# Kernel optimization log

Hardware: AMD Instinct MI355X
Metric: run time of the kernel (lower is better)

## Reference

```python
import jax, jax.numpy as jnp
import numpy as np

B, S, D = 2, 512, 128      # batch, seq_len, d_att
DG, NG = 64, 2             # d_group, n_group = D // DG


def setup_inputs() -> dict:
    key = jax.random.key(0)
    ks = jax.random.split(key, 12)
    def w(k, shape, scale):
        return jax.random.normal(k, shape, dtype=jnp.float32) * scale
    proj_scale = 1.0 / D                      # xavier_uniform-ish std / sqrt(d_att)
    mlp1 = (2.0 / (DG + DG)) ** 0.5
    mlp2 = (2.0 / (DG + 16)) ** 0.5
    mlp3 = (2.0 / (16 + 1)) ** 0.5
    return {
        "x": w(ks[0], (B, S, D), 1.0),
        "positional_adding_bias": w(ks[1], (1, NG, 1, S, S), 1.0),
        "positional_multiplying_bias": jax.random.uniform(ks[2], (1, NG, 1, S, S), dtype=jnp.float32),
        "Wq": w(ks[3], (D, D), proj_scale),
        "Wk": w(ks[4], (D, D), proj_scale),
        "Wv": w(ks[5], (D, D), proj_scale),
        "W1": w(ks[6], (DG, DG), mlp1), "b1": jnp.zeros((DG,), jnp.float32),
        "W2": w(ks[7], (DG, 16), mlp2), "b2": jnp.zeros((16,), jnp.float32),
        "W3": w(ks[8], (16, 1), mlp3),  "b3": jnp.zeros((1,), jnp.float32),
    }


def reference(x, positional_adding_bias, positional_multiplying_bias,
              Wq, Wk, Wv, W1, b1, W2, b2, W3, b3):
    Q = x @ Wq   # [B,S,D]
    K = x @ Wk
    V = x @ Wv
    # pairwise Q-K differences, grouped: [B,S,S,NG,DG] (d_att split as n_group,d_group)
    diff = (Q[:, :, None, :] - K[:, None, :, :]).reshape(B, S, S, NG, DG)
    # per-group scoring MLP (Linear->ReLU x3, final width 1)
    h = jax.nn.relu(diff @ W1 + b1)
    h = jax.nn.relu(h @ W2 + b2)
    a = jax.nn.relu(h @ W3 + b3)                 # [B,S,S,NG,1]
    a = jnp.transpose(a, (0, 3, 4, 1, 2))        # [B,NG,1,S,S]
    a = a * positional_multiplying_bias + positional_adding_bias
    a = jax.nn.softmax(a, axis=-1)[:, :, 0]      # [B,NG,S,S], softmax over keys
    # NOTE: original reshapes V as (d_group, n_group) — faithful reproduction
    Vr = V.reshape(B, S, DG, NG)                 # [B,S,DG,NG]
    out = jnp.einsum('bisk,bkji->bsji', a, Vr)   # [B,S,DG,NG]
    return out.reshape(B, S, D)
```

## Files before the change

kernel.cpp:

```cpp
#include <hip/hip_runtime.h>

#define BQ 2
#define SQ 512
#define DQ 128
#define DGQ 64
#define NGQ 2

typedef float float2v __attribute__((ext_vector_type(2)));


__global__ __launch_bounds__(256) void proj_kernel(
    const float* __restrict__ x,
    const float* __restrict__ Wq, const float* __restrict__ Wk,
    const float* __restrict__ Wv,
    const float* __restrict__ W1, const float* __restrict__ b1,
    float* __restrict__ QW1, float* __restrict__ KW1, float* __restrict__ Vp)
{
    const int t = threadIdx.x;
    const int row = blockIdx.x;
    __shared__ float xs[DQ];
    __shared__ float part[3][2][DQ];
    __shared__ float qs[DQ], ks[DQ];

    if (t < DQ) xs[t] = x[(size_t)row * DQ + t];
    __syncthreads();

    const int f = t & 127, h = t >> 7;
    float aq = 0.f, ak = 0.f, av = 0.f;
    const int d0 = h * 64;
    #pragma unroll 8
    for (int d = 0; d < 64; ++d) {
        const float xv = xs[d0 + d];
        const size_t o = (size_t)(d0 + d) * DQ + f;
        aq = fmaf(xv, Wq[o], aq);
        ak = fmaf(xv, Wk[o], ak);
        av = fmaf(xv, Wv[o], av);
    }
    part[0][h][f] = aq; part[1][h][f] = ak; part[2][h][f] = av;
    __syncthreads();

    if (t < DQ) {
        qs[t] = part[0][0][t] + part[0][1][t];
        const float v = part[2][0][t] + part[2][1][t];
        Vp[((size_t)row * NGQ + (t & 1)) * DGQ + (t >> 1)] = v;
    } else {
        const int f2 = t - DQ;
        ks[f2] = part[1][0][f2] + part[1][1][f2];
    }
    __syncthreads();

    const int fb = t & 127, side = t >> 7;
    const int g = fb >> 6, c = fb & 63;
    const float* src = side ? ks : qs;
    float acc = side ? 0.f : b1[c];
    #pragma unroll 8
    for (int e = 0; e < 64; ++e)
        acc = fmaf(src[g * 64 + e], W1[e * DGQ + c], acc);
    (side ? KW1 : QW1)[(size_t)row * DQ + fb] = acc;
}

__global__ __launch_bounds__(512) void attn_kernel(
    const float* __restrict__ QW1, const float* __restrict__ KW1,
    const float* __restrict__ Vp,
    const float* __restrict__ W2, const float* __restrict__ b2,
    const float* __restrict__ W3, const float* __restrict__ b3,
    const float* __restrict__ pos_add, const float* __restrict__ pos_mul,
    float* __restrict__ out)
{
    const int t = threadIdx.x;
    const int ipair = blockIdx.x & 255;
    const int g = (blockIdx.x >> 8) & 1;
    const int b = blockIdx.x >> 9;
    const int i0 = ipair * 2;

    __shared__ __align__(16) float qsl[2][DGQ];
    __shared__ __align__(8)  float sc[SQ * 2];
    __shared__ float redm[2][8], reds[2][8];
    __shared__ float avs[2][8][DGQ];

    if (t < 2 * DGQ) {
        const int qq = t >> 6, e = t & 63;
        qsl[qq][e] = QW1[((size_t)(b * SQ + i0 + qq)) * DQ + g * DGQ + e];
    }
    const size_t bo0 = ((size_t)g * SQ + i0) * SQ + t;
    const float pm0 = pos_mul[bo0],      pa0 = pos_add[bo0];
    const float pm1 = pos_mul[bo0 + SQ], pa1 = pos_add[bo0 + SQ];
    __syncthreads();

    const float4* krow = reinterpret_cast<const float4*>(
        KW1 + ((size_t)(b * SQ + t)) * DQ + g * DGQ);
    const float4* qv0 = reinterpret_cast<const float4*>(&qsl[0][0]);
    const float4* qv1 = reinterpret_cast<const float4*>(&qsl[1][0]);
    const float2v* b2v = reinterpret_cast<const float2v*>(b2);
    const float2v zero2 = {0.f, 0.f};

    float2v acc0[8], acc1[8];
    #pragma unroll
    for (int o = 0; o < 8; ++o) { acc0[o] = b2v[o]; acc1[o] = b2v[o]; }

    float4 kva = krow[0], kvb = krow[1];
    #pragma unroll
    for (int grp = 0; grp < 8; ++grp) {
        float4 nka, nkb;
        if (grp < 7) { nka = krow[grp * 2 + 2]; nkb = krow[grp * 2 + 3]; }
        #pragma unroll
        for (int u = 0; u < 2; ++u) {
            const int c4 = grp * 2 + u;
            const float4 kv = u ? kvb : kva;
            const float4 qa = qv0[c4], qb = qv1[c4];
            const float2v k01 = {kv.x, kv.y}, k23 = {kv.z, kv.w};
            const float2v ha01 = __builtin_elementwise_max(
                float2v{qa.x, qa.y} - k01, zero2);
            const float2v ha23 = __builtin_elementwise_max(
                float2v{qa.z, qa.w} - k23, zero2);
            const float2v hb01 = __builtin_elementwise_max(
                float2v{qb.x, qb.y} - k01, zero2);
            const float2v hb23 = __builtin_elementwise_max(
                float2v{qb.z, qb.w} - k23, zero2);
            const float2v* w2r = reinterpret_cast<const float2v*>(W2 + c4 * 64);
            #pragma unroll
            for (int o = 0; o < 8; ++o) {
                const float2v w0 = w2r[o],      w1 = w2r[8 + o];
                const float2v w2_ = w2r[16 + o], w3_ = w2r[24 + o];
                acc0[o] += ha01.x * w0;  acc0[o] += ha01.y * w1;
                acc0[o] += ha23.x * w2_; acc0[o] += ha23.y * w3_;
                acc1[o] += hb01.x * w0;  acc1[o] += hb01.y * w1;
                acc1[o] += hb23.x * w2_; acc1[o] += hb23.y * w3_;
            }
        }
        kva = nka; kvb = nkb;
    }
    float a0 = b3[0], a1 = b3[0];
    #pragma unroll
    for (int o = 0; o < 8; ++o) {
        a0 = fmaf(fmaxf(acc0[o].x, 0.f), W3[2 * o], a0);
        a0 = fmaf(fmaxf(acc0[o].y, 0.f), W3[2 * o + 1], a0);
        a1 = fmaf(fmaxf(acc1[o].x, 0.f), W3[2 * o], a1);
        a1 = fmaf(fmaxf(acc1[o].y, 0.f), W3[2 * o + 1], a1);
    }
    const float logit0 = fmaf(fmaxf(a0, 0.f), pm0, pa0);
    const float logit1 = fmaf(fmaxf(a1, 0.f), pm1, pa1);

    float m0 = logit0, m1 = logit1;
    #pragma unroll
    for (int off = 32; off > 0; off >>= 1) {
        m0 = fmaxf(m0, __shfl_xor(m0, off));
        m1 = fmaxf(m1, __shfl_xor(m1, off));
    }
    const int wave = t >> 6;
    if ((t & 63) == 0) { redm[0][wave] = m0; redm[1][wave] = m1; }
    __syncthreads();
    float M0 = redm[0][0], M1 = redm[1][0];
    #pragma unroll
    for (int w = 1; w < 8; ++w) {
        M0 = fmaxf(M0, redm[0][w]); M1 = fmaxf(M1, redm[1][w]);
    }
    const float e0 = __expf(logit0 - M0);
    const float e1 = __expf(logit1 - M1);
    *reinterpret_cast<float2v*>(&sc[t * 2]) = float2v{e0, e1};
    float s0 = e0, s1 = e1;
    #pragma unroll
    for (int off = 32; off > 0; off >>= 1) {
        s0 += __shfl_xor(s0, off);
        s1 += __shfl_xor(s1, off);
    }
    if ((t & 63) == 0) { reds[0][wave] = s0; reds[1][wave] = s1; }
    __syncthreads();
    float S0 = 0.f, S1 = 0.f;
    #pragma unroll
    for (int w = 0; w < 8; ++w) { S0 += reds[0][w]; S1 += reds[1][w]; }
    const float inv0 = 1.f / S0, inv1 = 1.f / S1;

    const int dim = t & 63, q = t >> 6;
    const float* vbase = Vp + (((size_t)(b * SQ + q * 64)) * NGQ + g) * DGQ + dim;
    float2v accv = {0.f, 0.f};
    #pragma unroll 16
    for (int k = 0; k < 64; ++k) {
        const float v = vbase[(size_t)k * (NGQ * DGQ)];
        const float2v sv = *reinterpret_cast<const float2v*>(&sc[(q * 64 + k) * 2]);
        accv += v * sv;
    }
    avs[0][q][dim] = accv.x;
    avs[1][q][dim] = accv.y;
    __syncthreads();
    if (t < 2 * DGQ) {
        const int qq = t >> 6, d = t & 63;
        float sum = 0.f;
        #pragma unroll
        for (int w = 0; w < 8; ++w) sum += avs[qq][w][d];
        out[((size_t)(b * SQ + i0 + qq)) * DQ + d * NGQ + g] =
            sum * (qq ? inv1 : inv0);
    }
}

extern "C" void kernel_launch(void* const* d_in, const int* in_sizes, int n_in,
                              void* d_out, int out_size, void* d_ws, size_t ws_size,
                              hipStream_t stream) {
    const float* x       = (const float*)d_in[0];
    const float* pos_add = (const float*)d_in[1];
    const float* pos_mul = (const float*)d_in[2];
    const float* Wq      = (const float*)d_in[3];
    const float* Wk      = (const float*)d_in[4];
    const float* Wv      = (const float*)d_in[5];
    const float* W1      = (const float*)d_in[6];
    const float* b1      = (const float*)d_in[7];
    const float* W2      = (const float*)d_in[8];
    const float* b2      = (const float*)d_in[9];
    const float* W3      = (const float*)d_in[10];
    const float* b3      = (const float*)d_in[11];
    float* out = (float*)d_out;

    float* ws  = (float*)d_ws;
    float* QW1 = ws;
    float* KW1 = ws + 131072;
    float* Vp  = ws + 262144;

    proj_kernel<<<BQ * SQ, 256, 0, stream>>>(x, Wq, Wk, Wv, W1, b1,
                                             QW1, KW1, Vp);
    attn_kernel<<<BQ * NGQ * SQ / 2, 512, 0, stream>>>(QW1, KW1, Vp, W2, b2,
                                                       W3, b3, pos_add, pos_mul,
                                                       out);
}
```

Before: 118.7 us.

## Compute scoring MLP layer 2 with split-bf16 MFMA and four queries per block

Replaces the per-thread scalar FMA evaluation of the 64->16 MLP layer with 16x16x32 bf16 MFMA instructions. A three-term hi/lo bf16 split keeps near-fp32 accuracy. Each block now handles four query rows instead of two, so K rows and W2 fragments are reused across more queries, and the grid shrinks by half. The softmax and the PV stage are reorganized with vectorized pos-bias loads and four-wide probability buffers. This trades extra MFMA passes and shuffle reductions for far fewer VALU FMAs.

```diff
diff --git a/kernel.cpp b/kernel.cpp
--- a/kernel.cpp
+++ b/kernel.cpp
@@ -6,7 +6,8 @@
 #define DGQ 64
 #define NGQ 2
 
-typedef float float2v __attribute__((ext_vector_type(2)));
+typedef float f32x4 __attribute__((ext_vector_type(4)));
+typedef __bf16 bf16x8 __attribute__((ext_vector_type(8)));
 
 
 __global__ __launch_bounds__(256) void proj_kernel(
@@ -59,7 +60,7 @@
     (side ? KW1 : QW1)[(size_t)row * DQ + fb] = acc;
 }
 
-__global__ __launch_bounds__(512) void attn_kernel(
+__global__ __launch_bounds__(512, 4) void attn_kernel(
     const float* __restrict__ QW1, const float* __restrict__ KW1,
     const float* __restrict__ Vp,
     const float* __restrict__ W2, const float* __restrict__ b2,
@@ -68,128 +69,156 @@
     float* __restrict__ out)
 {
     const int t = threadIdx.x;
-    const int ipair = blockIdx.x & 255;
-    const int g = (blockIdx.x >> 8) & 1;
-    const int b = blockIdx.x >> 9;
-    const int i0 = ipair * 2;
-
-    __shared__ __align__(16) float qsl[2][DGQ];
-    __shared__ __align__(8)  float sc[SQ * 2];
-    __shared__ float redm[2][8], reds[2][8];
-    __shared__ float avs[2][8][DGQ];
-
-    if (t < 2 * DGQ) {
-        const int qq = t >> 6, e = t & 63;
-        qsl[qq][e] = QW1[((size_t)(b * SQ + i0 + qq)) * DQ + g * DGQ + e];
-    }
-    const size_t bo0 = ((size_t)g * SQ + i0) * SQ + t;
-    const float pm0 = pos_mul[bo0],      pa0 = pos_add[bo0];
-    const float pm1 = pos_mul[bo0 + SQ], pa1 = pos_add[bo0 + SQ];
-    __syncthreads();
-
-    const float4* krow = reinterpret_cast<const float4*>(
-        KW1 + ((size_t)(b * SQ + t)) * DQ + g * DGQ);
-    const float4* qv0 = reinterpret_cast<const float4*>(&qsl[0][0]);
-    const float4* qv1 = reinterpret_cast<const float4*>(&qsl[1][0]);
-    const float2v* b2v = reinterpret_cast<const float2v*>(b2);
-    const float2v zero2 = {0.f, 0.f};
-
-    float2v acc0[8], acc1[8];
-    #pragma unroll
-    for (int o = 0; o < 8; ++o) { acc0[o] = b2v[o]; acc1[o] = b2v[o]; }
-
-    float4 kva = krow[0], kvb = krow[1];
-    #pragma unroll
-    for (int grp = 0; grp < 8; ++grp) {
-        float4 nka, nkb;
-        if (grp < 7) { nka = krow[grp * 2 + 2]; nkb = krow[grp * 2 + 3]; }
+    const int lane = t & 63, w = t >> 6;
+    const int lg = lane >> 4, lr = lane & 15;
+    const int ib = blockIdx.x & 127;
+    const int g  = (blockIdx.x >> 7) & 1;
+    const int b  = blockIdx.x >> 8;
+    const int i0 = ib * 4;
+
+    __shared__ __align__(16) float Qs[4][DGQ];
+    __shared__ __align__(16) float logits[4][SQ];
+    __shared__ __align__(16) float pbuf[SQ * 4];
+    __shared__ __align__(16) float avs[8][DGQ][4];
+    __shared__ float redm[4][2], reds[4][2];
+
+    if (t < 256) {
+        const int i = t >> 6, k = t & 63;
+        Qs[i][k] = QW1[((size_t)(b * SQ + i0 + i)) * DQ + g * DGQ + k];
+    }
+
+    bf16x8 bhf[2], blf[2];
+    #pragma unroll
+    for (int H = 0; H < 2; ++H) {
+        #pragma unroll
+        for (int e = 0; e < 8; ++e) {
+            const int k = H * 32 + (e >> 2) * 16 + lg * 4 + (e & 3);
+            const float wv = W2[k * 16 + lr];
+            const __bf16 hi = (__bf16)wv;
+            bhf[H][e] = hi;
+            blf[H][e] = (__bf16)(wv - (float)hi);
+        }
+    }
+    const float w3r = W3[lr];
+    const float b2r = b2[lr];
+    const float b3s = b3[0];
+
+    __syncthreads();
+
+    #pragma unroll
+    for (int pass = 0; pass < 2; ++pass) {
+        const int jb0 = w * 64 + pass * 32;
+        f32x4 kreg[2][4];
         #pragma unroll
         for (int u = 0; u < 2; ++u) {
-            const int c4 = grp * 2 + u;
-            const float4 kv = u ? kvb : kva;
-            const float4 qa = qv0[c4], qb = qv1[c4];
-            const float2v k01 = {kv.x, kv.y}, k23 = {kv.z, kv.w};
-            const float2v ha01 = __builtin_elementwise_max(
-                float2v{qa.x, qa.y} - k01, zero2);
-            const float2v ha23 = __builtin_elementwise_max(
-                float2v{qa.z, qa.w} - k23, zero2);
-            const float2v hb01 = __builtin_elementwise_max(
-                float2v{qb.x, qb.y} - k01, zero2);
-            const float2v hb23 = __builtin_elementwise_max(
-                float2v{qb.z, qb.w} - k23, zero2);
-            const float2v* w2r = reinterpret_cast<const float2v*>(W2 + c4 * 64);
+            const float* kr =
+                KW1 + ((size_t)(b * SQ + jb0 + u * 16 + lr)) * DQ + g * DGQ;
             #pragma unroll
-            for (int o = 0; o < 8; ++o) {
-                const float2v w0 = w2r[o],      w1 = w2r[8 + o];
-                const float2v w2_ = w2r[16 + o], w3_ = w2r[24 + o];
-                acc0[o] += ha01.x * w0;  acc0[o] += ha01.y * w1;
-                acc0[o] += ha23.x * w2_; acc0[o] += ha23.y * w3_;
-                acc1[o] += hb01.x * w0;  acc1[o] += hb01.y * w1;
-                acc1[o] += hb23.x * w2_; acc1[o] += hb23.y * w3_;
+            for (int c = 0; c < 4; ++c)
+                kreg[u][c] = *reinterpret_cast<const f32x4*>(
+                    kr + (c & 1) * 16 + (c >> 1) * 32 + lg * 4);
+        }
+        #pragma unroll
+        for (int i = 0; i < 4; ++i) {
+            f32x4 qf[4];
+            #pragma unroll
+            for (int c = 0; c < 4; ++c)
+                qf[c] = *reinterpret_cast<const f32x4*>(
+                    &Qs[i][(c & 1) * 16 + (c >> 1) * 32 + lg * 4]);
+            #pragma unroll
+            for (int u = 0; u < 2; ++u) {
+                f32x4 acc = {0.f, 0.f, 0.f, 0.f};
+                #pragma unroll
+                for (int H = 0; H < 2; ++H) {
+                    bf16x8 ah, al;
+                    #pragma unroll
+                    for (int cc = 0; cc < 2; ++cc) {
+                        const int c = H * 2 + cc;
+                        #pragma unroll
+                        for (int e = 0; e < 4; ++e) {
+                            const float hv =
+                                fmaxf(qf[c][e] - kreg[u][c][e], 0.f);
+                            const __bf16 hb = (__bf16)hv;
+                            ah[cc * 4 + e] = hb;
+                            al[cc * 4 + e] = (__bf16)(hv - (float)hb);
+                        }
+                    }
+                    acc = __builtin_amdgcn_mfma_f32_16x16x32_bf16(
+                        ah, bhf[H], acc, 0, 0, 0);
+                    acc = __builtin_amdgcn_mfma_f32_16x16x32_bf16(
+                        al, bhf[H], acc, 0, 0, 0);
+                    acc = __builtin_amdgcn_mfma_f32_16x16x32_bf16(
+                        ah, blf[H], acc, 0, 0, 0);
+                }
+                float s0 = fmaxf(acc[0] + b2r, 0.f) * w3r;
+                float s1 = fmaxf(acc[1] + b2r, 0.f) * w3r;
+                float s2 = fmaxf(acc[2] + b2r, 0.f) * w3r;
+                float s3 = fmaxf(acc[3] + b2r, 0.f) * w3r;
+                #pragma unroll
+                for (int off = 1; off < 16; off <<= 1) {
+                    s0 += __shfl_xor(s0, off);
+                    s1 += __shfl_xor(s1, off);
+                    s2 += __shfl_xor(s2, off);
+                    s3 += __shfl_xor(s3, off);
+                }
+                if (lr == 0) {
+                    f32x4 sv = {s0, s1, s2, s3};
+                    *reinterpret_cast<f32x4*>(
+                        &logits[i][jb0 + u * 16 + lg * 4]) = sv;
+                }
             }
         }
-        kva = nka; kvb = nkb;
-    }
-    float a0 = b3[0], a1 = b3[0];
-    #pragma unroll
-    for (int o = 0; o < 8; ++o) {
-        a0 = fmaf(fmaxf(acc0[o].x, 0.f), W3[2 * o], a0);
-        a0 = fmaf(fmaxf(acc0[o].y, 0.f), W3[2 * o + 1], a0);
-        a1 = fmaf(fmaxf(acc1[o].x, 0.f), W3[2 * o], a1);
-        a1 = fmaf(fmaxf(acc1[o].y, 0.f), W3[2 * o + 1], a1);
-    }
-    const float logit0 = fmaf(fmaxf(a0, 0.f), pm0, pa0);
-    const float logit1 = fmaf(fmaxf(a1, 0.f), pm1, pa1);
-
-    float m0 = logit0, m1 = logit1;
-    #pragma unroll
-    for (int off = 32; off > 0; off >>= 1) {
-        m0 = fmaxf(m0, __shfl_xor(m0, off));
-        m1 = fmaxf(m1, __shfl_xor(m1, off));
-    }
-    const int wave = t >> 6;
-    if ((t & 63) == 0) { redm[0][wave] = m0; redm[1][wave] = m1; }
-    __syncthreads();
-    float M0 = redm[0][0], M1 = redm[1][0];
-    #pragma unroll
-    for (int w = 1; w < 8; ++w) {
-        M0 = fmaxf(M0, redm[0][w]); M1 = fmaxf(M1, redm[1][w]);
-    }
-    const float e0 = __expf(logit0 - M0);
-    const float e1 = __expf(logit1 - M1);
-    *reinterpret_cast<float2v*>(&sc[t * 2]) = float2v{e0, e1};
-    float s0 = e0, s1 = e1;
-    #pragma unroll
-    for (int off = 32; off > 0; off >>= 1) {
-        s0 += __shfl_xor(s0, off);
-        s1 += __shfl_xor(s1, off);
-    }
-    if ((t & 63) == 0) { reds[0][wave] = s0; reds[1][wave] = s1; }
-    __syncthreads();
-    float S0 = 0.f, S1 = 0.f;
-    #pragma unroll
-    for (int w = 0; w < 8; ++w) { S0 += reds[0][w]; S1 += reds[1][w]; }
-    const float inv0 = 1.f / S0, inv1 = 1.f / S1;
-
-    const int dim = t & 63, q = t >> 6;
-    const float* vbase = Vp + (((size_t)(b * SQ + q * 64)) * NGQ + g) * DGQ + dim;
-    float2v accv = {0.f, 0.f};
-    #pragma unroll 16
-    for (int k = 0; k < 64; ++k) {
-        const float v = vbase[(size_t)k * (NGQ * DGQ)];
-        const float2v sv = *reinterpret_cast<const float2v*>(&sc[(q * 64 + k) * 2]);
-        accv += v * sv;
-    }
-    avs[0][q][dim] = accv.x;
-    avs[1][q][dim] = accv.y;
-    __syncthreads();
-    if (t < 2 * DGQ) {
-        const int qq = t >> 6, d = t & 63;
+    }
+    __syncthreads();
+
+    const int si = w >> 1, hf = w & 1;
+    const int qi = i0 + si;
+    const int j0 = hf * 256 + lane * 4;
+    const f32x4 raw = *reinterpret_cast<const f32x4*>(&logits[si][j0]);
+    const size_t po = ((size_t)(g * SQ + qi)) * SQ + j0;
+    const f32x4 pm4 = *reinterpret_cast<const f32x4*>(pos_mul + po);
+    const f32x4 pa4 = *reinterpret_cast<const f32x4*>(pos_add + po);
+    f32x4 lgt;
+    #pragma unroll
+    for (int c = 0; c < 4; ++c)
+        lgt[c] = fmaf(fmaxf(raw[c] + b3s, 0.f), pm4[c], pa4[c]);
+    float m = fmaxf(fmaxf(lgt[0], lgt[1]), fmaxf(lgt[2], lgt[3]));
+    #pragma unroll
+    for (int off = 1; off < 64; off <<= 1) m = fmaxf(m, __shfl_xor(m, off));
+    if (lane == 0) redm[si][hf] = m;
+    __syncthreads();
+    const float M = fmaxf(redm[si][0], redm[si][1]);
+    f32x4 e4;
+    float ls = 0.f;
+    #pragma unroll
+    for (int c = 0; c < 4; ++c) { e4[c] = __expf(lgt[c] - M); ls += e4[c]; }
+    #pragma unroll
+    for (int c = 0; c < 4; ++c) pbuf[(j0 + c) * 4 + si] = e4[c];
+    #pragma unroll
+    for (int off = 1; off < 64; off <<= 1) ls += __shfl_xor(ls, off);
+    if (lane == 0) reds[si][hf] = ls;
+    __syncthreads();
+
+    f32x4 av = {0.f, 0.f, 0.f, 0.f};
+    const float* vb =
+        Vp + (((size_t)(b * SQ + w * 64)) * NGQ + g) * DGQ + lane;
+    #pragma unroll 8
+    for (int n = 0; n < 64; ++n) {
+        const float v = vb[(size_t)n * (NGQ * DGQ)];
+        const f32x4 p4 =
+            *reinterpret_cast<const f32x4*>(&pbuf[(w * 64 + n) * 4]);
+        av += v * p4;
+    }
+    *reinterpret_cast<f32x4*>(&avs[w][lane][0]) = av;
+    __syncthreads();
+
+    if (t < 256) {
+        const int i2 = t >> 6, d = t & 63;
         float sum = 0.f;
         #pragma unroll
-        for (int w = 0; w < 8; ++w) sum += avs[qq][w][d];
-        out[((size_t)(b * SQ + i0 + qq)) * DQ + d * NGQ + g] =
-            sum * (qq ? inv1 : inv0);
+        for (int ww = 0; ww < 8; ++ww) sum += avs[ww][d][i2];
+        const float den = reds[i2][0] + reds[i2][1];
+        out[((size_t)(b * SQ + i0 + i2)) * DQ + d * NGQ + g] = sum / den;
     }
 }
 
@@ -217,7 +246,7 @@
 
     proj_kernel<<<BQ * SQ, 256, 0, stream>>>(x, Wq, Wk, Wv, W1, b1,
                                              QW1, KW1, Vp);
-    attn_kernel<<<BQ * NGQ * SQ / 2, 512, 0, stream>>>(QW1, KW1, Vp, W2, b2,
+    attn_kernel<<<BQ * NGQ * SQ / 4, 512, 0, stream>>>(QW1, KW1, Vp, W2, b2,
                                                        W3, b3, pos_add, pos_mul,
                                                        out);
 }
```

After: 112.3 us. 1.06x faster.
